# Kernel optimization log

Measured on AMD Instinct MI355X. Metric: run time of the kernel, lower is better.

## Reference

```python
import jax, jax.numpy as jnp
import numpy as np

B, CIN, H, W = 32, 2048, 14, 14
D, K, NCLASS = 128, 32, 1000
WIN = 5
BN_EPS = 1e-5


def setup_inputs() -> dict:
    key = jax.random.key(0)
    ks = jax.random.split(key, 6)
    std = 1.0 / np.sqrt(K * D)  # Encoding codeword init range
    x = jax.random.normal(ks[0], (B, CIN, H, W), jnp.float32)
    conv_w = jax.random.normal(ks[1], (D, CIN), jnp.float32) * 0.02
    conv_b = jnp.zeros((D,), jnp.float32)
    bn_gamma = jnp.ones((D,), jnp.float32)
    bn_beta = jnp.zeros((D,), jnp.float32)
    bn_mean = jnp.zeros((D,), jnp.float32)
    bn_var = jnp.ones((D,), jnp.float32)
    codewords = jax.random.uniform(ks[2], (K, D), jnp.float32, -std, std)
    # Encoding smoothing factors init uniform(-1, 0)
    scale = -jax.random.uniform(ks[3], (K,), jnp.float32)
    cls_w = jax.random.normal(ks[4], (NCLASS, K * D), jnp.float32) * 0.01
    cls_b = jnp.zeros((NCLASS,), jnp.float32)
    return dict(x=x, conv_w=conv_w, conv_b=conv_b, bn_gamma=bn_gamma,
                bn_beta=bn_beta, bn_mean=bn_mean, bn_var=bn_var,
                codewords=codewords, scale=scale, cls_w=cls_w, cls_b=cls_b)


def reference(x, conv_w, conv_b, bn_gamma, bn_beta, bn_mean, bn_var,
              codewords, scale, cls_w, cls_b):
    # 1x1 conv + BN(eval) + ReLU are pointwise -> apply once on the full map
    y = jnp.einsum('bchw,dc->bdhw', x, conv_w) + conv_b[None, :, None, None]
    inv = bn_gamma / jnp.sqrt(bn_var + BN_EPS)
    y = (y - bn_mean[None, :, None, None]) * inv[None, :, None, None] \
        + bn_beta[None, :, None, None]
    y = jax.nn.relu(y)

    # all 5x5 sliding windows, stride 1 -> P = ph*pw patches, N = 25 pixels
    ph, pw = H - WIN + 1, W - WIN + 1
    pat = jnp.stack([y[:, :, i:i + ph, j:j + pw]
                     for i in range(WIN) for j in range(WIN)], axis=2)
    # [B, D, N, ph, pw] -> [B, P, N, D]
    X = pat.reshape(B, D, WIN * WIN, ph * pw).transpose(0, 3, 2, 1)

    # soft-VQ Encoding: scaled L2 dists, softmax assign over K, residual aggregate
    x2 = jnp.sum(X * X, -1)                               # [B,P,N]
    c2 = jnp.sum(codewords * codewords, -1)               # [K]
    xc = jnp.einsum('bpnd,kd->bpnk', X, codewords)        # [B,P,N,K]
    dist = x2[..., None] - 2.0 * xc + c2                  # ||x - c||^2
    A = jax.nn.softmax(scale * dist, axis=-1)             # scale < 0
    E = jnp.einsum('bpnk,bpnd->bpkd', A, X) \
        - jnp.einsum('bpnk,kd->bpkd', A, codewords)       # [B,P,K,D]

    # View(-1, K*D) + L2 Normalize per patch, then sum over patches
    e = E.reshape(B, ph * pw, K * D)
    e = e / jnp.maximum(jnp.linalg.norm(e, axis=-1, keepdims=True), 1e-12)
    v = jnp.sum(e, axis=1)                                # [B, K*D]
    return v @ cls_w.T + cls_b
```

## Files before the change

kernel.cpp:

```cpp
#include <hip/hip_runtime.h>
#include <math.h>

#define NB 32
#define CIN 2048
#define HH 14
#define WW 14
#define HW 196
#define DD 128
#define KK 32
#define NCLASS 1000
#define PWN 10
#define NP 100
#define NPIX 25
#define KD 4096
#define BN_EPS 1e-5f
#define YELEMS (NB * HW * DD)
#define MTOT (NB * HW)
#define MT 128
#define KS 16

__global__ __launch_bounds__(256) void k_wt(const float* __restrict__ cw,
                                            float* __restrict__ wt) {
  __shared__ float T[32][33];
  const int tx = threadIdx.x & 31;
  const int ty = threadIdx.x >> 5;
  const int c0 = blockIdx.x * 32;
  const int d0 = blockIdx.y * 32;
  #pragma unroll
  for (int k = 0; k < 4; ++k)
    T[ty + 8 * k][tx] = cw[(size_t)(d0 + ty + 8 * k) * CIN + c0 + tx];
  __syncthreads();
  #pragma unroll
  for (int k = 0; k < 4; ++k)
    wt[(size_t)(c0 + ty + 8 * k) * DD + d0 + tx] = T[tx][ty + 8 * k];
}

__global__ __launch_bounds__(256) void k_conv(const float* __restrict__ x,
                                              const float* __restrict__ wt,
                                              float* __restrict__ y_part,
                                              int cspl) {
  __shared__ float Xs[2][KS][132];
  __shared__ float Ws[2][KS][132];

  const int t = threadIdx.x;
  const int m0 = blockIdx.x * MT;
  const int s = blockIdx.y;
  const int c0 = s * cspl;
  const int nsteps = cspl / KS;

  const int sr = t >> 4;
  const int sc = (t & 15) * 8;
  const int msb = m0 + sc;
  const int b0i = msb / HW, h0 = msb - b0i * HW;
  const int m2 = msb + 4;
  const int b1i = m2 / HW, h1 = m2 - b1i * HW;
  const float* xp1 = x + (size_t)b0i * CIN * HW + (size_t)(c0 + sr) * HW + h0;
  const float* xp2 = x + (size_t)b1i * CIN * HW + (size_t)(c0 + sr) * HW + h1;
  const float* wp  = wt + (size_t)(c0 + sr) * DD + sc;

  const int pg = t >> 4;
  const int dg = t & 15;
  const int pa = pg * 4;
  const int da = dg * 4;

  float4 acc[2][2][4];
  #pragma unroll
  for (int pi = 0; pi < 2; ++pi)
    #pragma unroll
    for (int di = 0; di < 2; ++di)
      #pragma unroll
      for (int i = 0; i < 4; ++i)
        acc[pi][di][i] = make_float4(0.f, 0.f, 0.f, 0.f);

  {
    float4 xv1 = *(const float4*)xp1;
    float4 xv2 = *(const float4*)xp2;
    float4 wv1 = *(const float4*)wp;
    float4 wv2 = *(const float4*)(wp + 4);
    *(float4*)&Xs[0][sr][sc]     = xv1;
    *(float4*)&Xs[0][sr][sc + 4] = xv2;
    *(float4*)&Ws[0][sr][sc]     = wv1;
    *(float4*)&Ws[0][sr][sc + 4] = wv2;
  }
  __syncthreads();

  for (int ks = 0; ks < nsteps; ++ks) {
    const int cur = ks & 1;
    float4 xv1, xv2, wv1, wv2;
    const bool more = (ks + 1 < nsteps);
    if (more) {
      const size_t coff = (size_t)(ks + 1) * KS * HW;
      const size_t woff = (size_t)(ks + 1) * KS * DD;
      xv1 = *(const float4*)(xp1 + coff);
      xv2 = *(const float4*)(xp2 + coff);
      wv1 = *(const float4*)(wp + woff);
      wv2 = *(const float4*)(wp + woff + 4);
    }
    #pragma unroll
    for (int c = 0; c < KS; ++c) {
      float4 xa = *(const float4*)&Xs[cur][c][pa];
      float4 xb = *(const float4*)&Xs[cur][c][pa + 64];
      float4 wa = *(const float4*)&Ws[cur][c][da];
      float4 wb = *(const float4*)&Ws[cur][c][da + 64];
      float xs0[4] = {xa.x, xa.y, xa.z, xa.w};
      float xs1[4] = {xb.x, xb.y, xb.z, xb.w};
      #pragma unroll
      for (int i = 0; i < 4; ++i) {
        acc[0][0][i].x += xs0[i] * wa.x; acc[0][0][i].y += xs0[i] * wa.y;
        acc[0][0][i].z += xs0[i] * wa.z; acc[0][0][i].w += xs0[i] * wa.w;
        acc[0][1][i].x += xs0[i] * wb.x; acc[0][1][i].y += xs0[i] * wb.y;
        acc[0][1][i].z += xs0[i] * wb.z; acc[0][1][i].w += xs0[i] * wb.w;
        acc[1][0][i].x += xs1[i] * wa.x; acc[1][0][i].y += xs1[i] * wa.y;
        acc[1][0][i].z += xs1[i] * wa.z; acc[1][0][i].w += xs1[i] * wa.w;
        acc[1][1][i].x += xs1[i] * wb.x; acc[1][1][i].y += xs1[i] * wb.y;
        acc[1][1][i].z += xs1[i] * wb.z; acc[1][1][i].w += xs1[i] * wb.w;
      }
    }
    if (more) {
      const int nxt = cur ^ 1;
      *(float4*)&Xs[nxt][sr][sc]     = xv1;
      *(float4*)&Xs[nxt][sr][sc + 4] = xv2;
      *(float4*)&Ws[nxt][sr][sc]     = wv1;
      *(float4*)&Ws[nxt][sr][sc + 4] = wv2;
    }
    __syncthreads();
  }

  float* yp = y_part + (size_t)s * YELEMS + (size_t)m0 * DD;
  #pragma unroll
  for (int pi = 0; pi < 2; ++pi)
    #pragma unroll
    for (int i = 0; i < 4; ++i) {
      const int row = pa + pi * 64 + i;
      #pragma unroll
      for (int di = 0; di < 2; ++di)
        *(float4*)(yp + (size_t)row * DD + da + di * 64) = acc[pi][di][i];
    }
}

__global__ __launch_bounds__(256) void k_bnred(const float* __restrict__ y_part,
    float* __restrict__ y, const float* __restrict__ convb,
    const float* __restrict__ gamma, const float* __restrict__ beta,
    const float* __restrict__ mean, const float* __restrict__ var,
    int nsplit) {
  int idx = blockIdx.x * 256 + threadIdx.x;
  float4 a = *(const float4*)&y_part[(size_t)idx * 4];
  for (int s = 1; s < nsplit; ++s) {
    float4 p = *(const float4*)&y_part[(size_t)s * YELEMS + (size_t)idx * 4];
    a.x += p.x; a.y += p.y; a.z += p.z; a.w += p.w;
  }
  int d4 = (idx * 4) & (DD - 1);
  float o[4] = {a.x, a.y, a.z, a.w};
  #pragma unroll
  for (int j = 0; j < 4; ++j) {
    int d = d4 + j;
    float inv = gamma[d] * rsqrtf(var[d] + BN_EPS);
    float val = (o[j] + convb[d] - mean[d]) * inv + beta[d];
    o[j] = fmaxf(val, 0.f);
  }
  *(float4*)&y[(size_t)idx * 4] = make_float4(o[0], o[1], o[2], o[3]);
}

__global__ __launch_bounds__(256) void k_encode(const float* __restrict__ y,
    const float* __restrict__ codewords, const float* __restrict__ scale,
    float* __restrict__ v) {
  __shared__ float Xs[NPIX][132];
  __shared__ float cws[KK][132];
  __shared__ float cwT[DD][36];
  __shared__ float Am[NPIX][36];
  __shared__ float x2s[NPIX];
  __shared__ float sks[KK];
  __shared__ float c2s[KK];
  __shared__ float scs[KK];
  __shared__ float red[5];

  const int t = threadIdx.x;
  const int bp = blockIdx.x;
  const int b = bp / NP;
  const int p = bp - b * NP;
  const int pi = p / PWN, pj = p - pi * PWN;
  const int wave = t >> 6, lane = t & 63;

  #pragma unroll
  for (int i = 0; i < 4; ++i) {
    int idx = t + 256 * i;
    if (idx < NPIX * 32) {
      int n = idx >> 5;
      int d4 = (idx & 31) * 4;
      int di = n / 5, dj = n - di * 5;
      int hw = (pi + di) * WW + (pj + dj);
      float4 vx = *(const float4*)&y[((size_t)b * HW + hw) * DD + d4];
      *(float4*)&Xs[n][d4] = vx;
    }
    int k = idx >> 5;
    int d4 = (idx & 31) * 4;
    float4 vc = *(const float4*)&codewords[k * DD + d4];
    *(float4*)&cws[k][d4] = vc;
  }
  __syncthreads();

  #pragma unroll
  for (int i = 0; i < 4; ++i) {
    int idx = t + 256 * i;
    int k = idx & 31;
    int d4 = (idx >> 5) * 4;
    float4 vc = *(const float4*)&cws[k][d4];
    cwT[d4 + 0][k] = vc.x; cwT[d4 + 1][k] = vc.y;
    cwT[d4 + 2][k] = vc.z; cwT[d4 + 3][k] = vc.w;
  }
  for (int n = wave; n < NPIX; n += 4) {
    float a = Xs[n][lane];
    float c = Xs[n][lane + 64];
    float r = a * a + c * c;
    #pragma unroll
    for (int off = 32; off; off >>= 1) r += __shfl_xor(r, off, 64);
    if (lane == 0) x2s[n] = r;
  }
  if (t < KK) {
    float s = 0.f;
    #pragma unroll 8
    for (int d4 = 0; d4 < DD; d4 += 4) {
      float4 c4 = *(const float4*)&cws[t][d4];
      s += c4.x * c4.x + c4.y * c4.y + c4.z * c4.z + c4.w * c4.w;
    }
    c2s[t] = s;
    scs[t] = scale[t];
  }
  __syncthreads();

  {
    const int n = t >> 3;
    const int k0 = (t & 7) * 4;
    if (n < NPIX) {
      float a0 = 0.f, a1 = 0.f, a2 = 0.f, a3 = 0.f;
      #pragma unroll 8
      for (int d4 = 0; d4 < DD; d4 += 4) {
        float4 xv = *(const float4*)&Xs[n][d4];
        float4 c0 = *(const float4*)&cwT[d4 + 0][k0];
        float4 c1 = *(const float4*)&cwT[d4 + 1][k0];
        float4 c2 = *(const float4*)&cwT[d4 + 2][k0];
        float4 c3 = *(const float4*)&cwT[d4 + 3][k0];
        a0 += xv.x * c0.x + xv.y * c1.x + xv.z * c2.x + xv.w * c3.x;
        a1 += xv.x * c0.y + xv.y * c1.y + xv.z * c2.y + xv.w * c3.y;
        a2 += xv.x * c0.z + xv.y * c1.z + xv.z * c2.z + xv.w * c3.z;
        a3 += xv.x * c0.w + xv.y * c1.w + xv.z * c2.w + xv.w * c3.w;
      }
      float x2 = x2s[n];
      float l0 = scs[k0 + 0] * (x2 - 2.f * a0 + c2s[k0 + 0]);
      float l1 = scs[k0 + 1] * (x2 - 2.f * a1 + c2s[k0 + 1]);
      float l2 = scs[k0 + 2] * (x2 - 2.f * a2 + c2s[k0 + 2]);
      float l3 = scs[k0 + 3] * (x2 - 2.f * a3 + c2s[k0 + 3]);
      float m = fmaxf(fmaxf(l0, l1), fmaxf(l2, l3));
      m = fmaxf(m, __shfl_xor(m, 1));
      m = fmaxf(m, __shfl_xor(m, 2));
      m = fmaxf(m, __shfl_xor(m, 4));
      float e0 = __expf(l0 - m), e1 = __expf(l1 - m);
      float e2 = __expf(l2 - m), e3 = __expf(l3 - m);
      float s = e0 + e1 + e2 + e3;
      s += __shfl_xor(s, 1);
      s += __shfl_xor(s, 2);
      s += __shfl_xor(s, 4);
      float inv = 1.f / s;
      *(float4*)&Am[n][k0] =
          make_float4(e0 * inv, e1 * inv, e2 * inv, e3 * inv);
    }
  }
  __syncthreads();

  if (t < KK) {
    float s = 0.f;
    #pragma unroll
    for (int n = 0; n < NPIX; ++n) s += Am[n][t];
    sks[t] = s;
  }
  __syncthreads();

  const int dd = (t & 63) * 2;
  const int k0 = (t >> 6) * 8;
  float ea[8][2];
  #pragma unroll
  for (int kk = 0; kk < 8; ++kk) { ea[kk][0] = 0.f; ea[kk][1] = 0.f; }
  #pragma unroll 5
  for (int n = 0; n < NPIX; ++n) {
    float2 xv = *(const float2*)&Xs[n][dd];
    float4 q0 = *(const float4*)&Am[n][k0];
    float4 q1 = *(const float4*)&Am[n][k0 + 4];
    float av[8] = {q0.x, q0.y, q0.z, q0.w, q1.x, q1.y, q1.z, q1.w};
    #pragma unroll
    for (int kk = 0; kk < 8; ++kk) {
      ea[kk][0] += av[kk] * xv.x;
      ea[kk][1] += av[kk] * xv.y;
    }
  }
  float ss = 0.f;
  #pragma unroll
  for (int kk = 0; kk < 8; ++kk) {
    int k = k0 + kk;
    float s = sks[k];
    float2 cv = *(const float2*)&cws[k][dd];
    ea[kk][0] -= s * cv.x;
    ea[kk][1] -= s * cv.y;
    ss += ea[kk][0] * ea[kk][0] + ea[kk][1] * ea[kk][1];
  }
  #pragma unroll
  for (int off = 32; off; off >>= 1) ss += __shfl_xor(ss, off, 64);
  if (lane == 0) red[wave] = ss;
  __syncthreads();
  if (t == 0) {
    float tot = red[0] + red[1] + red[2] + red[3];
    red[4] = 1.f / fmaxf(sqrtf(tot), 1e-12f);
  }
  __syncthreads();
  float rn = red[4];
  float* vb = v + (size_t)b * KD;
  #pragma unroll
  for (int kk = 0; kk < 8; ++kk) {
    int k = k0 + kk;
    atomicAdd(&vb[k * DD + dd + 0], ea[kk][0] * rn);
    atomicAdd(&vb[k * DD + dd + 1], ea[kk][1] * rn);
  }
}

__global__ __launch_bounds__(256) void k_cls(const float* __restrict__ v,
    const float* __restrict__ cls_w, const float* __restrict__ cls_b,
    float* __restrict__ out) {
  const int wave = threadIdx.x >> 6;
  const int lane = threadIdx.x & 63;
  const int n0 = blockIdx.x * 8 + wave * 2;
  const float* w0 = cls_w + (size_t)n0 * KD;
  const float* w1 = cls_w + (size_t)(n0 + 1) * KD;
  float acc0[NB], acc1[NB];
  #pragma unroll
  for (int b = 0; b < NB; ++b) { acc0[b] = 0.f; acc1[b] = 0.f; }
  #pragma unroll 2
  for (int i = 0; i < 16; ++i) {
    int kd = i * 256 + lane * 4;
    float4 a4 = *(const float4*)&w0[kd];
    float4 b4 = *(const float4*)&w1[kd];
    #pragma unroll
    for (int b = 0; b < NB; ++b) {
      float4 v4 = *(const float4*)&v[b * KD + kd];
      acc0[b] += a4.x * v4.x + a4.y * v4.y + a4.z * v4.z + a4.w * v4.w;
      acc1[b] += b4.x * v4.x + b4.y * v4.y + b4.z * v4.z + b4.w * v4.w;
    }
  }
  #pragma unroll
  for (int b = 0; b < NB; ++b) {
    float r0 = acc0[b], r1 = acc1[b];
    #pragma unroll
    for (int off = 32; off; off >>= 1) {
      r0 += __shfl_xor(r0, off, 64);
      r1 += __shfl_xor(r1, off, 64);
    }
    if (lane == 0) {
      out[b * NCLASS + n0]     = r0 + cls_b[n0];
      out[b * NCLASS + n0 + 1] = r1 + cls_b[n0 + 1];
    }
  }
}

extern "C" void kernel_launch(void* const* d_in, const int* in_sizes, int n_in,
                              void* d_out, int out_size, void* d_ws, size_t ws_size,
                              hipStream_t stream) {
  const float* x         = (const float*)d_in[0];
  const float* conv_w    = (const float*)d_in[1];
  const float* conv_b    = (const float*)d_in[2];
  const float* bn_gamma  = (const float*)d_in[3];
  const float* bn_beta   = (const float*)d_in[4];
  const float* bn_mean   = (const float*)d_in[5];
  const float* bn_var    = (const float*)d_in[6];
  const float* codewords = (const float*)d_in[7];
  const float* scale     = (const float*)d_in[8];
  const float* cls_w     = (const float*)d_in[9];
  const float* cls_b     = (const float*)d_in[10];
  float* out = (float*)d_out;

  const size_t FIXED = ((size_t)CIN * DD + (size_t)YELEMS + (size_t)NB * KD)
                       * sizeof(float);
  int ksplit = 2;
  if (ws_size >= FIXED + 16 * (size_t)YELEMS * sizeof(float)) ksplit = 16;
  else if (ws_size >= FIXED + 8 * (size_t)YELEMS * sizeof(float)) ksplit = 8;
  else if (ws_size >= FIXED + 4 * (size_t)YELEMS * sizeof(float)) ksplit = 4;
  const int cspl = CIN / ksplit;

  float* wt     = (float*)d_ws;
  float* y_part = wt + (size_t)CIN * DD;
  float* y      = y_part + (size_t)ksplit * YELEMS;
  float* v      = y + (size_t)YELEMS;

  hipMemsetAsync(v, 0, (size_t)NB * KD * sizeof(float), stream);

  k_wt<<<dim3(CIN / 32, DD / 32), 256, 0, stream>>>(conv_w, wt);
  k_conv<<<dim3(MTOT / MT, ksplit), 256, 0, stream>>>(x, wt, y_part, cspl);
  k_bnred<<<YELEMS / (256 * 4), 256, 0, stream>>>(
      y_part, y, conv_b, bn_gamma, bn_beta, bn_mean, bn_var, ksplit);
  k_encode<<<NB * NP, 256, 0, stream>>>(y, codewords, scale, v);
  k_cls<<<NCLASS / 8, 256, 0, stream>>>(v, cls_w, cls_b, out);
}
```

Before: 333.8 us.

## Process multiple patches per encode block and replace atomics with partial-sum reduction

Each encode block now loops over several patches of one batch item, accumulating normalized residuals in registers. Each block writes its per-block partial to a scratch buffer, and a new reduction kernel sums the partials, replacing the 3200-block atomicAdd scheme and the memset. This amortizes the codeword load and transpose per block and removes atomic contention on v. The cost is fewer blocks (800), an extra kernel launch, and scratch space reused from the conv partials.

```diff
diff --git a/kernel.cpp b/kernel.cpp
--- a/kernel.cpp
+++ b/kernel.cpp
@@ -163,7 +163,7 @@
 
 __global__ __launch_bounds__(256) void k_encode(const float* __restrict__ y,
     const float* __restrict__ codewords, const float* __restrict__ scale,
-    float* __restrict__ v) {
+    float* __restrict__ vpart, int ppb) {
   __shared__ float Xs[NPIX][132];
   __shared__ float cws[KK][132];
   __shared__ float cwT[DD][36];
@@ -175,30 +175,18 @@
   __shared__ float red[5];
 
   const int t = threadIdx.x;
-  const int bp = blockIdx.x;
-  const int b = bp / NP;
-  const int p = bp - b * NP;
-  const int pi = p / PWN, pj = p - pi * PWN;
+  const int part = blockIdx.x;
+  const int b = blockIdx.y;
   const int wave = t >> 6, lane = t & 63;
 
   #pragma unroll
   for (int i = 0; i < 4; ++i) {
     int idx = t + 256 * i;
-    if (idx < NPIX * 32) {
-      int n = idx >> 5;
-      int d4 = (idx & 31) * 4;
-      int di = n / 5, dj = n - di * 5;
-      int hw = (pi + di) * WW + (pj + dj);
-      float4 vx = *(const float4*)&y[((size_t)b * HW + hw) * DD + d4];
-      *(float4*)&Xs[n][d4] = vx;
-    }
     int k = idx >> 5;
     int d4 = (idx & 31) * 4;
-    float4 vc = *(const float4*)&codewords[k * DD + d4];
-    *(float4*)&cws[k][d4] = vc;
+    *(float4*)&cws[k][d4] = *(const float4*)&codewords[k * DD + d4];
   }
   __syncthreads();
-
   #pragma unroll
   for (int i = 0; i < 4; ++i) {
     int idx = t + 256 * i;
@@ -208,14 +196,6 @@
     cwT[d4 + 0][k] = vc.x; cwT[d4 + 1][k] = vc.y;
     cwT[d4 + 2][k] = vc.z; cwT[d4 + 3][k] = vc.w;
   }
-  for (int n = wave; n < NPIX; n += 4) {
-    float a = Xs[n][lane];
-    float c = Xs[n][lane + 64];
-    float r = a * a + c * c;
-    #pragma unroll
-    for (int off = 32; off; off >>= 1) r += __shfl_xor(r, off, 64);
-    if (lane == 0) x2s[n] = r;
-  }
   if (t < KK) {
     float s = 0.f;
     #pragma unroll 8
@@ -226,99 +206,149 @@
     c2s[t] = s;
     scs[t] = scale[t];
   }
-  __syncthreads();
-
-  {
-    const int n = t >> 3;
-    const int k0 = (t & 7) * 4;
-    if (n < NPIX) {
-      float a0 = 0.f, a1 = 0.f, a2 = 0.f, a3 = 0.f;
-      #pragma unroll 8
-      for (int d4 = 0; d4 < DD; d4 += 4) {
-        float4 xv = *(const float4*)&Xs[n][d4];
-        float4 c0 = *(const float4*)&cwT[d4 + 0][k0];
-        float4 c1 = *(const float4*)&cwT[d4 + 1][k0];
-        float4 c2 = *(const float4*)&cwT[d4 + 2][k0];
-        float4 c3 = *(const float4*)&cwT[d4 + 3][k0];
-        a0 += xv.x * c0.x + xv.y * c1.x + xv.z * c2.x + xv.w * c3.x;
-        a1 += xv.x * c0.y + xv.y * c1.y + xv.z * c2.y + xv.w * c3.y;
-        a2 += xv.x * c0.z + xv.y * c1.z + xv.z * c2.z + xv.w * c3.z;
-        a3 += xv.x * c0.w + xv.y * c1.w + xv.z * c2.w + xv.w * c3.w;
+
+  const int dd = (t & 63) * 2;
+  const int k06 = (t >> 6) * 8;
+  float vacc[8][2];
+  #pragma unroll
+  for (int kk = 0; kk < 8; ++kk) { vacc[kk][0] = 0.f; vacc[kk][1] = 0.f; }
+
+  for (int pp = 0; pp < ppb; ++pp) {
+    const int p = part * ppb + pp;
+    if (p >= NP) break;
+    const int pi = p / PWN, pj = p - pi * PWN;
+
+    __syncthreads();
+    #pragma unroll
+    for (int i = 0; i < 4; ++i) {
+      int idx = t + 256 * i;
+      if (idx < NPIX * 32) {
+        int n = idx >> 5;
+        int d4 = (idx & 31) * 4;
+        int di = n / 5, dj = n - di * 5;
+        int hw = (pi + di) * WW + (pj + dj);
+        *(float4*)&Xs[n][d4] =
+            *(const float4*)&y[((size_t)b * HW + hw) * DD + d4];
       }
-      float x2 = x2s[n];
-      float l0 = scs[k0 + 0] * (x2 - 2.f * a0 + c2s[k0 + 0]);
-      float l1 = scs[k0 + 1] * (x2 - 2.f * a1 + c2s[k0 + 1]);
-      float l2 = scs[k0 + 2] * (x2 - 2.f * a2 + c2s[k0 + 2]);
-      float l3 = scs[k0 + 3] * (x2 - 2.f * a3 + c2s[k0 + 3]);
-      float m = fmaxf(fmaxf(l0, l1), fmaxf(l2, l3));
-      m = fmaxf(m, __shfl_xor(m, 1));
-      m = fmaxf(m, __shfl_xor(m, 2));
-      m = fmaxf(m, __shfl_xor(m, 4));
-      float e0 = __expf(l0 - m), e1 = __expf(l1 - m);
-      float e2 = __expf(l2 - m), e3 = __expf(l3 - m);
-      float s = e0 + e1 + e2 + e3;
-      s += __shfl_xor(s, 1);
-      s += __shfl_xor(s, 2);
-      s += __shfl_xor(s, 4);
-      float inv = 1.f / s;
-      *(float4*)&Am[n][k0] =
-          make_float4(e0 * inv, e1 * inv, e2 * inv, e3 * inv);
-    }
-  }
-  __syncthreads();
-
-  if (t < KK) {
-    float s = 0.f;
-    #pragma unroll
-    for (int n = 0; n < NPIX; ++n) s += Am[n][t];
-    sks[t] = s;
-  }
-  __syncthreads();
-
-  const int dd = (t & 63) * 2;
-  const int k0 = (t >> 6) * 8;
-  float ea[8][2];
-  #pragma unroll
-  for (int kk = 0; kk < 8; ++kk) { ea[kk][0] = 0.f; ea[kk][1] = 0.f; }
-  #pragma unroll 5
-  for (int n = 0; n < NPIX; ++n) {
-    float2 xv = *(const float2*)&Xs[n][dd];
-    float4 q0 = *(const float4*)&Am[n][k0];
-    float4 q1 = *(const float4*)&Am[n][k0 + 4];
-    float av[8] = {q0.x, q0.y, q0.z, q0.w, q1.x, q1.y, q1.z, q1.w};
+    }
+    __syncthreads();
+
+    for (int n = wave; n < NPIX; n += 4) {
+      float a = Xs[n][lane];
+      float c = Xs[n][lane + 64];
+      float r = a * a + c * c;
+      #pragma unroll
+      for (int off = 32; off; off >>= 1) r += __shfl_xor(r, off, 64);
+      if (lane == 0) x2s[n] = r;
+    }
+    __syncthreads();
+
+    {
+      const int n = t >> 3;
+      const int k0 = (t & 7) * 4;
+      if (n < NPIX) {
+        float a0 = 0.f, a1 = 0.f, a2 = 0.f, a3 = 0.f;
+        #pragma unroll 8
+        for (int d4 = 0; d4 < DD; d4 += 4) {
+          float4 xv = *(const float4*)&Xs[n][d4];
+          float4 c0 = *(const float4*)&cwT[d4 + 0][k0];
+          float4 c1 = *(const float4*)&cwT[d4 + 1][k0];
+          float4 c2 = *(const float4*)&cwT[d4 + 2][k0];
+          float4 c3 = *(const float4*)&cwT[d4 + 3][k0];
+          a0 += xv.x * c0.x + xv.y * c1.x + xv.z * c2.x + xv.w * c3.x;
+          a1 += xv.x * c0.y + xv.y * c1.y + xv.z * c2.y + xv.w * c3.y;
+          a2 += xv.x * c0.z + xv.y * c1.z + xv.z * c2.z + xv.w * c3.z;
+          a3 += xv.x * c0.w + xv.y * c1.w + xv.z * c2.w + xv.w * c3.w;
+        }
+        float x2 = x2s[n];
+        float l0 = scs[k0 + 0] * (x2 - 2.f * a0 + c2s[k0 + 0]);
+        float l1 = scs[k0 + 1] * (x2 - 2.f * a1 + c2s[k0 + 1]);
+        float l2 = scs[k0 + 2] * (x2 - 2.f * a2 + c2s[k0 + 2]);
+        float l3 = scs[k0 + 3] * (x2 - 2.f * a3 + c2s[k0 + 3]);
+        float m = fmaxf(fmaxf(l0, l1), fmaxf(l2, l3));
+        m = fmaxf(m, __shfl_xor(m, 1));
+        m = fmaxf(m, __shfl_xor(m, 2));
+        m = fmaxf(m, __shfl_xor(m, 4));
+        float e0 = __expf(l0 - m), e1 = __expf(l1 - m);
+        float e2 = __expf(l2 - m), e3 = __expf(l3 - m);
+        float s = e0 + e1 + e2 + e3;
+        s += __shfl_xor(s, 1);
+        s += __shfl_xor(s, 2);
+        s += __shfl_xor(s, 4);
+        float inv = 1.f / s;
+        *(float4*)&Am[n][k0] =
+            make_float4(e0 * inv, e1 * inv, e2 * inv, e3 * inv);
+      }
+    }
+    __syncthreads();
+
+    if (t < KK) {
+      float s = 0.f;
+      #pragma unroll
+      for (int n = 0; n < NPIX; ++n) s += Am[n][t];
+      sks[t] = s;
+    }
+    __syncthreads();
+
+    float ea[8][2];
+    #pragma unroll
+    for (int kk = 0; kk < 8; ++kk) { ea[kk][0] = 0.f; ea[kk][1] = 0.f; }
+    #pragma unroll 5
+    for (int n = 0; n < NPIX; ++n) {
+      float2 xv = *(const float2*)&Xs[n][dd];
+      float4 q0 = *(const float4*)&Am[n][k06];
+      float4 q1 = *(const float4*)&Am[n][k06 + 4];
+      float av[8] = {q0.x, q0.y, q0.z, q0.w, q1.x, q1.y, q1.z, q1.w};
+      #pragma unroll
+      for (int kk = 0; kk < 8; ++kk) {
+        ea[kk][0] += av[kk] * xv.x;
+        ea[kk][1] += av[kk] * xv.y;
+      }
+    }
+    float ss = 0.f;
     #pragma unroll
     for (int kk = 0; kk < 8; ++kk) {
-      ea[kk][0] += av[kk] * xv.x;
-      ea[kk][1] += av[kk] * xv.y;
-    }
-  }
-  float ss = 0.f;
-  #pragma unroll
-  for (int kk = 0; kk < 8; ++kk) {
-    int k = k0 + kk;
-    float s = sks[k];
-    float2 cv = *(const float2*)&cws[k][dd];
-    ea[kk][0] -= s * cv.x;
-    ea[kk][1] -= s * cv.y;
-    ss += ea[kk][0] * ea[kk][0] + ea[kk][1] * ea[kk][1];
-  }
-  #pragma unroll
-  for (int off = 32; off; off >>= 1) ss += __shfl_xor(ss, off, 64);
-  if (lane == 0) red[wave] = ss;
-  __syncthreads();
-  if (t == 0) {
-    float tot = red[0] + red[1] + red[2] + red[3];
-    red[4] = 1.f / fmaxf(sqrtf(tot), 1e-12f);
-  }
-  __syncthreads();
-  float rn = red[4];
-  float* vb = v + (size_t)b * KD;
-  #pragma unroll
-  for (int kk = 0; kk < 8; ++kk) {
-    int k = k0 + kk;
-    atomicAdd(&vb[k * DD + dd + 0], ea[kk][0] * rn);
-    atomicAdd(&vb[k * DD + dd + 1], ea[kk][1] * rn);
-  }
+      int k = k06 + kk;
+      float s = sks[k];
+      float2 cv = *(const float2*)&cws[k][dd];
+      ea[kk][0] -= s * cv.x;
+      ea[kk][1] -= s * cv.y;
+      ss += ea[kk][0] * ea[kk][0] + ea[kk][1] * ea[kk][1];
+    }
+    #pragma unroll
+    for (int off = 32; off; off >>= 1) ss += __shfl_xor(ss, off, 64);
+    if (lane == 0) red[wave] = ss;
+    __syncthreads();
+    if (t == 0) {
+      float tot = red[0] + red[1] + red[2] + red[3];
+      red[4] = 1.f / fmaxf(sqrtf(tot), 1e-12f);
+    }
+    __syncthreads();
+    float rn = red[4];
+    #pragma unroll
+    for (int kk = 0; kk < 8; ++kk) {
+      vacc[kk][0] += ea[kk][0] * rn;
+      vacc[kk][1] += ea[kk][1] * rn;
+    }
+  }
+
+  float* vp = vpart + ((size_t)part * NB + b) * KD;
+  #pragma unroll
+  for (int kk = 0; kk < 8; ++kk)
+    *(float2*)&vp[(k06 + kk) * DD + dd] =
+        make_float2(vacc[kk][0], vacc[kk][1]);
+}
+
+__global__ __launch_bounds__(256) void k_vred(const float* __restrict__ vpart,
+                                              float* __restrict__ v,
+                                              int npart) {
+  int idx = blockIdx.x * 256 + threadIdx.x;
+  float4 a = make_float4(0.f, 0.f, 0.f, 0.f);
+  for (int pt = 0; pt < npart; ++pt) {
+    float4 p = *(const float4*)&vpart[(size_t)pt * NB * KD + (size_t)idx * 4];
+    a.x += p.x; a.y += p.y; a.z += p.z; a.w += p.w;
+  }
+  *(float4*)&v[(size_t)idx * 4] = a;
 }
 
 __global__ __launch_bounds__(256) void k_cls(const float* __restrict__ v,
@@ -375,25 +405,34 @@
   const float* cls_b     = (const float*)d_in[10];
   float* out = (float*)d_out;
 
-  const size_t FIXED = ((size_t)CIN * DD + (size_t)YELEMS + (size_t)NB * KD)
-                       * sizeof(float);
-  int ksplit = 2;
-  if (ws_size >= FIXED + 16 * (size_t)YELEMS * sizeof(float)) ksplit = 16;
-  else if (ws_size >= FIXED + 8 * (size_t)YELEMS * sizeof(float)) ksplit = 8;
-  else if (ws_size >= FIXED + 4 * (size_t)YELEMS * sizeof(float)) ksplit = 4;
+  auto need = [](int kspl, int npart) -> size_t {
+    size_t scratch = (size_t)kspl * YELEMS;
+    size_t vp = (size_t)npart * NB * KD;
+    if (vp > scratch) scratch = vp;
+    return ((size_t)CIN * DD + scratch + (size_t)YELEMS
+            + (size_t)NB * KD) * sizeof(float);
+  };
+  int ksplit, npart;
+  if      (ws_size >= need(16, 25)) { ksplit = 16; npart = 25; }
+  else if (ws_size >= need(8, 25))  { ksplit = 8;  npart = 25; }
+  else if (ws_size >= need(4, 25))  { ksplit = 4;  npart = 25; }
+  else                              { ksplit = 2;  npart = 10; }
   const int cspl = CIN / ksplit;
-
-  float* wt     = (float*)d_ws;
-  float* y_part = wt + (size_t)CIN * DD;
-  float* y      = y_part + (size_t)ksplit * YELEMS;
-  float* v      = y + (size_t)YELEMS;
-
-  hipMemsetAsync(v, 0, (size_t)NB * KD * sizeof(float), stream);
+  const int ppb = (NP + npart - 1) / npart;
+  size_t scratchf = (size_t)ksplit * YELEMS;
+  if ((size_t)npart * NB * KD > scratchf) scratchf = (size_t)npart * NB * KD;
+
+  float* wt      = (float*)d_ws;
+  float* scratch = wt + (size_t)CIN * DD;
+  float* y       = scratch + scratchf;
+  float* v       = y + (size_t)YELEMS;
 
   k_wt<<<dim3(CIN / 32, DD / 32), 256, 0, stream>>>(conv_w, wt);
-  k_conv<<<dim3(MTOT / MT, ksplit), 256, 0, stream>>>(x, wt, y_part, cspl);
+  k_conv<<<dim3(MTOT / MT, ksplit), 256, 0, stream>>>(x, wt, scratch, cspl);
   k_bnred<<<YELEMS / (256 * 4), 256, 0, stream>>>(
-      y_part, y, conv_b, bn_gamma, bn_beta, bn_mean, bn_var, ksplit);
-  k_encode<<<NB * NP, 256, 0, stream>>>(y, codewords, scale, v);
+      scratch, y, conv_b, bn_gamma, bn_beta, bn_mean, bn_var, ksplit);
+  k_encode<<<dim3(npart, NB), 256, 0, stream>>>(y, codewords, scale,
+                                                scratch, ppb);
+  k_vred<<<NB * KD / (256 * 4), 256, 0, stream>>>(scratch, v, npart);
   k_cls<<<NCLASS / 8, 256, 0, stream>>>(v, cls_w, cls_b, out);
 }
```

Result: faster. 295.8 us (-11.4%).
